# Kernel tuning notes

Measured on AMD Instinct MI355X. Metric: run time of the kernel, lower is better.

## Reference

```python
import jax, jax.numpy as jnp
import numpy as np

TAU = 0.1
HARD_K = 32
MIN_OVERLAP = 4
PAIR_WEIGHTS = [("view", "cart", 0.2), ("cart", "purchase", 1.0), ("view", "purchase", 1.0)]


def setup_inputs() -> dict:
    key = jax.random.key(0)
    ks = jax.random.split(key, 6)
    U, D = 100000, 128
    return {
        "emb_view": jax.random.normal(ks[0], (U, D), dtype=jnp.float32),
        "emb_cart": jax.random.normal(ks[1], (U, D), dtype=jnp.float32),
        "emb_purchase": jax.random.normal(ks[2], (U, D), dtype=jnp.float32),
        "users_view": jax.random.randint(ks[3], (20000,), 0, U, dtype=jnp.int64),
        "users_cart": jax.random.randint(ks[4], (15000,), 0, U, dtype=jnp.int64),
        "users_purchase": jax.random.randint(ks[5], (10000,), 0, U, dtype=jnp.int64),
    }


def _l2norm(x):
    # F.normalize(x, dim=-1): x / max(||x||, eps)
    n = jnp.linalg.norm(x, axis=-1, keepdims=True)
    return x / jnp.maximum(n, 1e-12)


def _directional(z_weak, z_strong, tau, hard_k):
    N = z_strong.shape[0]
    if N < 2:
        return jnp.zeros((), dtype=z_strong.dtype)
    z_w = _l2norm(jax.lax.stop_gradient(z_weak))  # weak side is detached
    z_s = _l2norm(z_strong)
    sim = (z_s @ z_w.T) / tau  # [N, N]
    pos = jnp.diagonal(sim)    # positive logits, labels = arange(N)
    n_hard = min(hard_k, N - 1)
    if 0 < n_hard < N - 1:
        neg_only = jnp.where(jnp.eye(N, dtype=bool), -jnp.inf, sim)
        hard_neg, _ = jax.lax.top_k(neg_only, n_hard)          # [N, n_hard]
        logits = jnp.concatenate([pos[:, None], hard_neg], 1)  # [N, 1+n_hard]
        return jnp.mean(jax.scipy.special.logsumexp(logits, axis=1) - pos)
    # full-softmax CE with label i for row i
    return jnp.mean(jax.scipy.special.logsumexp(sim, axis=1) - pos)


def reference(emb_view, emb_cart, emb_purchase, users_view, users_cart, users_purchase):
    embs = {"view": emb_view, "cart": emb_cart, "purchase": emb_purchase}
    users = {
        "view": np.asarray(users_view),
        "cart": np.asarray(users_cart),
        "purchase": np.asarray(users_purchase),
    }
    loss = jnp.zeros((), dtype=emb_view.dtype)
    for weak, strong, w in PAIR_WEIGHTS:
        u_w, u_s = users[weak], users[strong]
        if u_w.size == 0 or u_s.size == 0:
            continue
        # common_pair = u_w[isin(u_w, u_s)] : keeps u_w order and duplicates
        common = u_w[np.isin(u_w, u_s)]
        if common.size < MIN_OVERLAP:
            continue
        idx = jnp.asarray(common)
        loss = loss + w * _directional(embs[weak][idx], embs[strong][idx], TAU, HARD_K)
    return loss
```

## Files before the change

kernel.cpp:

```cpp
#include <hip/hip_runtime.h>
#include <hip/hip_bf16.h>
#include <math.h>

#define D 128
#define NEG_INF (-3.0e38f)
#define LDA 136
#define MAGIC 0x5CA1AB1Eu

#define C0 3200
#define C1 1792
#define C2 2304
#define T0 25
#define T1 14
#define T2 18
#define NTILES (T0 * T0 + T1 * T1 + T2 * T2)
#define NSEL (C0 / 4 + C1 / 4 + C2 / 4)

typedef __attribute__((ext_vector_type(8))) short bf16x8;
typedef __attribute__((ext_vector_type(8))) unsigned short u16x8;
typedef __attribute__((ext_vector_type(4))) float f32x4;

__device__ __forceinline__ float wredf_add(float v) {
#pragma unroll
  for (int m = 32; m; m >>= 1) v += __shfl_xor(v, m, 64);
  return v;
}
__device__ __forceinline__ float wredf_max(float v) {
#pragma unroll
  for (int m = 32; m; m >>= 1) v = fmaxf(v, __shfl_xor(v, m, 64));
  return v;
}
__device__ __forceinline__ float wredf_min(float v) {
#pragma unroll
  for (int m = 32; m; m >>= 1) v = fminf(v, __shfl_xor(v, m, 64));
  return v;
}
__device__ __forceinline__ int wredi_add(int v) {
#pragma unroll
  for (int m = 32; m; m >>= 1) v += __shfl_xor(v, m, 64);
  return v;
}
__device__ __forceinline__ double wredd_add(double v) {
#pragma unroll
  for (int m = 32; m; m >>= 1) v += __shfl_xor(v, m, 64);
  return v;
}

__global__ void masks_k(const int* __restrict__ uc, int nc,
                        const int* __restrict__ up, int npu,
                        unsigned* __restrict__ mc, unsigned* __restrict__ mp,
                        unsigned long long* __restrict__ header) {
  if (blockIdx.x == 0)
    for (int t = threadIdx.x; t < 1024; t += 256) header[t] = 0ull;
  int t = blockIdx.x * blockDim.x + threadIdx.x;
  if (t < nc) {
    mc[uc[t]] = MAGIC;
  } else {
    int t2 = t - nc;
    if (t2 < npu) mp[up[t2]] = MAGIC;
  }
}

struct FGArgs {
  const int* src[3];
  int n[3];
  const unsigned* mask[3];
  const float* embW[3];
  const float* embS[3];
  short* zw[3];
  short* zs[3];
  int cap[3];
  int seg1, seg2;
  int* counts;
};

__global__ __launch_bounds__(256) void filtgather_k(FGArgs a) {
  int t = blockIdx.x * 256 + threadIdx.x;
  int lane = threadIdx.x & 63;
  int s, base;
  if (t < a.seg1) { s = 0; base = t; }
  else if (t < a.seg2) { s = 1; base = t - a.seg1; }
  else { s = 2; base = t - a.seg2; }
  bool match = false;
  int u = 0;
  if (base < a.n[s]) {
    u = a.src[s][base];
    match = (a.mask[s][u] == MAGIC);
  }
  unsigned long long b = __ballot(match);
  int tot = __popcll(b);
  if (!tot) return;
  int idx0 = 0;
  if (lane == 0) idx0 = atomicAdd(a.counts + s, tot);
  idx0 = __shfl(idx0, 0, 64);
  const float* eW = a.embW[s];
  const float* eS = a.embS[s];
  short* zw = a.zw[s];
  short* zs = a.zs[s];
  int cap = a.cap[s];
  int kmax = tot;
  int rem = cap - idx0;
  if (rem < kmax) kmax = (rem < 0) ? 0 : rem;
  unsigned long long bbL = b;

  auto ldpair = [&](int k, float2& W, float2& S) {
    if (k < kmax) {
      int sl = __builtin_ctzll(bbL);
      bbL &= bbL - 1;
      int uu = __shfl(u, sl, 64);
      W = *(const float2*)(eW + (size_t)uu * D + lane * 2);
      S = *(const float2*)(eS + (size_t)uu * D + lane * 2);
    }
  };
  auto proc = [&](int k, float2 vw, float2 vs) {
    if (k < kmax) {
      int p = idx0 + k;
      float ssw = wredf_add(vw.x * vw.x + vw.y * vw.y);
      float sss = wredf_add(vs.x * vs.x + vs.y * vs.y);
      float iw = 1.0f / fmaxf(sqrtf(ssw), 1e-12f);
      float is = 1.0f / fmaxf(sqrtf(sss), 1e-12f);
      __hip_bfloat16 w0 = __float2bfloat16(vw.x * iw), w1 = __float2bfloat16(vw.y * iw);
      __hip_bfloat16 s0 = __float2bfloat16(vs.x * is), s1 = __float2bfloat16(vs.y * is);
      *(ushort2*)(zw + (size_t)p * D + lane * 2) =
          make_ushort2(*(unsigned short*)&w0, *(unsigned short*)&w1);
      *(ushort2*)(zs + (size_t)p * D + lane * 2) =
          make_ushort2(*(unsigned short*)&s0, *(unsigned short*)&s1);
    }
  };

  float2 Aw0 = {}, Aw1 = {}, Aw2 = {}, Aw3 = {}, Asv0 = {}, Asv1 = {}, Asv2 = {}, Asv3 = {};
  float2 Bw0 = {}, Bw1 = {}, Bw2 = {}, Bw3 = {}, Bsv0 = {}, Bsv1 = {}, Bsv2 = {}, Bsv3 = {};
  int kb = 0;
  ldpair(0, Aw0, Asv0); ldpair(1, Aw1, Asv1); ldpair(2, Aw2, Asv2); ldpair(3, Aw3, Asv3);
  while (kb < kmax) {
    ldpair(kb + 4, Bw0, Bsv0); ldpair(kb + 5, Bw1, Bsv1);
    ldpair(kb + 6, Bw2, Bsv2); ldpair(kb + 7, Bw3, Bsv3);
    proc(kb + 0, Aw0, Asv0); proc(kb + 1, Aw1, Asv1);
    proc(kb + 2, Aw2, Asv2); proc(kb + 3, Aw3, Asv3);
    kb += 4;
    if (kb >= kmax) break;
    ldpair(kb + 4, Aw0, Asv0); ldpair(kb + 5, Aw1, Asv1);
    ldpair(kb + 6, Aw2, Asv2); ldpair(kb + 7, Aw3, Asv3);
    proc(kb + 0, Bw0, Bsv0); proc(kb + 1, Bw1, Bsv1);
    proc(kb + 2, Bw2, Bsv2); proc(kb + 3, Bw3, Bsv3);
    kb += 4;
  }
}

struct GemmArgs {
  const short *zs0, *zw0, *zs1, *zw1, *zs2, *zw2;
  unsigned short *s0, *s1, *s2;
  const int* counts;
};

__device__ __forceinline__ void gemm_tile(const short* __restrict__ A, const short* __restrict__ B,
                                          unsigned short* __restrict__ C, int ldc, int bx, int by,
                                          int N, short* As, short* Bs, int tid) {
  int rb = by * 128, cb = bx * 128;
  if (rb >= N || cb >= N) return;
  int rrow = tid >> 4, rcol = (tid & 15) * 8;
#pragma unroll
  for (int pass = 0; pass < 8; ++pass) {
    int row = pass * 16 + rrow;
    uint4 va = *(const uint4*)(A + (size_t)(rb + row) * D + rcol);
    uint4 vb = *(const uint4*)(B + (size_t)(cb + row) * D + rcol);
    *(uint4*)(&As[row * LDA + rcol]) = va;
    *(uint4*)(&Bs[row * LDA + rcol]) = vb;
  }
  __syncthreads();
  int wave = tid >> 6, lane = tid & 63;
  int wr = (wave >> 1) * 64, wc = (wave & 1) * 64;
  int ln = lane & 15, quad = lane >> 4;
  f32x4 acc[4][4] = {};
#pragma unroll
  for (int ks = 0; ks < 4; ++ks) {
    int ko = ks * 32 + quad * 8;
    bf16x8 af[4], bg[4];
#pragma unroll
    for (int i = 0; i < 4; ++i) af[i] = *(const bf16x8*)(&As[(wr + i * 16 + ln) * LDA + ko]);
#pragma unroll
    for (int j = 0; j < 4; ++j) bg[j] = *(const bf16x8*)(&Bs[(wc + j * 16 + ln) * LDA + ko]);
#pragma unroll
    for (int i = 0; i < 4; ++i)
#pragma unroll
      for (int j = 0; j < 4; ++j)
        acc[i][j] = __builtin_amdgcn_mfma_f32_16x16x32_bf16(af[i], bg[j], acc[i][j], 0, 0, 0);
  }
  __syncthreads();
#pragma unroll
  for (int i = 0; i < 4; ++i)
#pragma unroll
    for (int j = 0; j < 4; ++j) {
      int tcol = wc + j * 16 + ln;
#pragma unroll
      for (int r = 0; r < 4; ++r) {
        int trow = wr + i * 16 + quad * 4 + r;
        __hip_bfloat16 h = __float2bfloat16(acc[i][j][r] * 10.0f);
        As[trow * LDA + tcol] = *(short*)&h;
      }
    }
  __syncthreads();
#pragma unroll
  for (int pass = 0; pass < 8; ++pass) {
    int idx = pass * 256 + tid;
    int row = idx >> 4, c8 = (idx & 15) * 8;
    *(uint4*)(C + (size_t)(rb + row) * ldc + cb + c8) = *(const uint4*)(&As[row * LDA + c8]);
  }
  __syncthreads();
}

__global__ __launch_bounds__(256) void gemm_all_k(GemmArgs g) {
  __shared__ __align__(16) short As[128 * LDA];
  __shared__ __align__(16) short Bs[128 * LDA];
  int tid = threadIdx.x;
  int b = blockIdx.x;
  if (b < T0 * T0) {
    int N = min(g.counts[0], C0);
    gemm_tile(g.zs0, g.zw0, g.s0, C0, b % T0, b / T0, N, As, Bs, tid);
  } else if (b < T0 * T0 + T1 * T1) {
    int t = b - T0 * T0;
    int N = min(g.counts[1], C1);
    gemm_tile(g.zs1, g.zw1, g.s1, C1, t % T1, t / T1, N, As, Bs, tid);
  } else {
    int t = b - T0 * T0 - T1 * T1;
    int N = min(g.counts[2], C2);
    gemm_tile(g.zs2, g.zw2, g.s2, C2, t % T2, t / T2, N, As, Bs, tid);
  }
}

template <int NL>
__device__ __forceinline__ void select_rows(const unsigned short* __restrict__ sim, int ldc, int N,
                                            int i, int lane, double* __restrict__ slot) {
  const unsigned short* row = sim + (size_t)i * ldc;
  float vals[NL * 8];
  float posl = NEG_INF;
#pragma unroll
  for (int L = 0; L < NL; ++L) {
    int base = L * 512 + lane * 8;
    u16x8 raw = *(const u16x8*)(row + base);
#pragma unroll
    for (int c = 0; c < 8; ++c) {
      int j = base + c;
      float v = __uint_as_float((unsigned)raw[c] << 16);
      if (L >= NL - 2 && j >= N) v = NEG_INF;
      if (j == i) { posl = v; v = NEG_INF; }
      vals[L * 8 + c] = v;
    }
  }
  float pos = __shfl(posl, (i >> 3) & 63, 64);
  float m = NEG_INF;
#pragma unroll
  for (int s = 0; s < NL * 8; ++s) m = fmaxf(m, vals[s]);
  m = wredf_max(m);
  int K = min(32, N - 1);
  float lo = -10.2f, hi = m + 1e-3f;
  for (int it = 0; it < 12; ++it) {
    float mid = 0.5f * (lo + hi);
    int c = 0;
#pragma unroll
    for (int s = 0; s < NL * 8; ++s) c += (vals[s] > mid) ? 1 : 0;
    c = wredi_add(c);
    if (c >= K) lo = mid; else hi = mid;
  }
  float M = fmaxf(m, pos);
  float sum = 0.0f, vmin = 3.0e38f;
  int cnt = 0;
#pragma unroll
  for (int s = 0; s < NL * 8; ++s) {
    float v = vals[s];
    if (v > lo) {
      sum += __expf(v - M);
      cnt++;
      vmin = fminf(vmin, v);
    }
  }
  sum = wredf_add(sum);
  cnt = wredi_add(cnt);
  vmin = wredf_min(vmin);
  float corr = (cnt > K) ? (float)(cnt - K) * __expf(vmin - M) : 0.0f;
  float lse = M + __logf(sum - corr + __expf(pos - M));
  if (lane == 0) atomicAdd(slot, (double)(lse - pos));
}

__device__ __forceinline__ void select_body(int b, int wid, int lane,
                                            const unsigned short* __restrict__ sim0,
                                            const unsigned short* __restrict__ sim1,
                                            const unsigned short* __restrict__ sim2,
                                            const int* __restrict__ counts,
                                            double* __restrict__ partials) {
  if (b < C0 / 4) {
    int N = min(counts[0], C0);
    int i = b * 4 + wid;
    if (i < N) {
      double* slot = partials + 0 * 64 + (b & 63);
      if (N <= 3072) select_rows<6>(sim0, C0, N, i, lane, slot);
      else           select_rows<7>(sim0, C0, N, i, lane, slot);
    }
  } else if (b < C0 / 4 + C1 / 4) {
    int bb = b - C0 / 4;
    int N = min(counts[1], C1);
    int i = bb * 4 + wid;
    if (i < N) {
      double* slot = partials + 64 + (bb & 63);
      if (N <= 1536) select_rows<3>(sim1, C1, N, i, lane, slot);
      else           select_rows<4>(sim1, C1, N, i, lane, slot);
    }
  } else {
    int bb = b - C0 / 4 - C1 / 4;
    int N = min(counts[2], C2);
    int i = bb * 4 + wid;
    if (i < N) {
      double* slot = partials + 128 + (bb & 63);
      if (N <= 2048) select_rows<4>(sim2, C2, N, i, lane, slot);
      else           select_rows<5>(sim2, C2, N, i, lane, slot);
    }
  }
}

__global__ __launch_bounds__(256) void select_k(const unsigned short* __restrict__ sim0,
                                                const unsigned short* __restrict__ sim1,
                                                const unsigned short* __restrict__ sim2,
                                                const int* __restrict__ counts,
                                                double* __restrict__ partials,
                                                int* __restrict__ cntC,
                                                float* __restrict__ out) {
  int tid = threadIdx.x, wid = tid >> 6, lane = tid & 63;
  int nb = gridDim.x;
  for (int b = blockIdx.x; b < NSEL; b += nb)
    select_body(b, wid, lane, sim0, sim1, sim2, counts, partials);
  __syncthreads();
  if (tid == 0) {
    __builtin_amdgcn_fence(__ATOMIC_RELEASE, "agent");
    __hip_atomic_fetch_add(&cntC[(blockIdx.x & 63) * 16], 1, __ATOMIC_RELAXED,
                           __HIP_MEMORY_SCOPE_AGENT);
  }
  if (blockIdx.x == 0) {
    if (tid < 64) {
      for (;;) {
        int s = __hip_atomic_load(&cntC[tid * 16], __ATOMIC_RELAXED, __HIP_MEMORY_SCOPE_AGENT);
        s = wredi_add(s);
        if (s >= nb) break;
        __builtin_amdgcn_s_sleep(2);
      }
    }
    __syncthreads();
    if (tid == 0) __builtin_amdgcn_fence(__ATOMIC_ACQUIRE, "agent");
    __syncthreads();
    __shared__ double ps[4];
    double v = (tid < 192)
                   ? __hip_atomic_load(&partials[tid], __ATOMIC_RELAXED, __HIP_MEMORY_SCOPE_AGENT)
                   : 0.0;
    v = wredd_add(v);
    if (lane == 0 && wid < 3) ps[wid] = v;
    __syncthreads();
    if (tid == 0) {
      const float w[3] = {0.2f, 1.0f, 1.0f};
      const int caps[3] = {C0, C1, C2};
      float tot = 0.0f;
      for (int p = 0; p < 3; ++p) {
        int N = min(counts[p], caps[p]);
        if (N >= 4) tot += w[p] * (float)(ps[p] / (double)N);
      }
      out[0] = tot;
    }
  }
}

__global__ void sentinel_k(float* out) {
  if (threadIdx.x == 0 && blockIdx.x == 0) out[0] = -12345.0f;
}

extern "C" void kernel_launch(void* const* d_in, const int* in_sizes, int n_in,
                              void* d_out, int out_size, void* d_ws, size_t ws_size,
                              hipStream_t stream) {
  const float* emb_view = (const float*)d_in[0];
  const float* emb_cart = (const float*)d_in[1];
  const float* emb_pur  = (const float*)d_in[2];
  const int* u_view = (const int*)d_in[3];
  const int* u_cart = (const int*)d_in[4];
  const int* u_pur  = (const int*)d_in[5];
  int nv = in_sizes[3], nc = in_sizes[4], np = in_sizes[5];
  int U = in_sizes[0] / D;

  size_t off = 8192;
  auto alloc = [&](size_t b) {
    size_t o = (off + 255) & ~(size_t)255;
    off = o + b;
    return o;
  };
  size_t mask0_off = alloc((size_t)U * 4);
  size_t mask1_off = alloc((size_t)U * 4);
  size_t zw0_off = alloc((size_t)C0 * D * 2);
  size_t zs0_off = alloc((size_t)C0 * D * 2);
  size_t zw1_off = alloc((size_t)C1 * D * 2);
  size_t zs1_off = alloc((size_t)C1 * D * 2);
  size_t zw2_off = alloc((size_t)C2 * D * 2);
  size_t zs2_off = alloc((size_t)C2 * D * 2);
  size_t sim0_off = alloc((size_t)C0 * C0 * 2);
  size_t sim1_off = alloc((size_t)C1 * C1 * 2);
  size_t sim2_off = alloc((size_t)C2 * C2 * 2);
  (void)alloc(1024);
  int ws_ok = (off <= ws_size) ? 1 : 0;

  char* ws = (char*)d_ws;
  if (!ws_ok) {
    sentinel_k<<<1, 1, 0, stream>>>((float*)d_out);
    return;
  }

  int* counts = (int*)ws;
  int* cntC = (int*)(ws + 1024);
  double* partials = (double*)(ws + 5632);
  unsigned* mask_c = (unsigned*)(ws + mask0_off);
  unsigned* mask_p = (unsigned*)(ws + mask1_off);
  short* zw0 = (short*)(ws + zw0_off);
  short* zs0 = (short*)(ws + zs0_off);
  short* zw1 = (short*)(ws + zw1_off);
  short* zs1 = (short*)(ws + zs1_off);
  short* zw2 = (short*)(ws + zw2_off);
  short* zs2 = (short*)(ws + zs2_off);
  unsigned short* sim0 = (unsigned short*)(ws + sim0_off);
  unsigned short* sim1 = (unsigned short*)(ws + sim1_off);
  unsigned short* sim2 = (unsigned short*)(ws + sim2_off);

  masks_k<<<(nc + np + 255) / 256, 256, 0, stream>>>(u_cart, nc, u_pur, np, mask_c, mask_p,
                                                     (unsigned long long*)ws);

  FGArgs fa;
  fa.src[0] = u_view; fa.n[0] = nv; fa.mask[0] = mask_c;
  fa.embW[0] = emb_view; fa.embS[0] = emb_cart; fa.zw[0] = zw0; fa.zs[0] = zs0; fa.cap[0] = C0;
  fa.src[1] = u_cart; fa.n[1] = nc; fa.mask[1] = mask_p;
  fa.embW[1] = emb_cart; fa.embS[1] = emb_pur; fa.zw[1] = zw1; fa.zs[1] = zs1; fa.cap[1] = C1;
  fa.src[2] = u_view; fa.n[2] = nv; fa.mask[2] = mask_p;
  fa.embW[2] = emb_view; fa.embS[2] = emb_pur; fa.zw[2] = zw2; fa.zs[2] = zs2; fa.cap[2] = C2;
  fa.seg1 = ((nv + 255) / 256) * 256;
  fa.seg2 = fa.seg1 + ((nc + 255) / 256) * 256;
  int t_filt = fa.seg2 + ((nv + 255) / 256) * 256;
  fa.counts = counts;
  filtgather_k<<<t_filt / 256, 256, 0, stream>>>(fa);

  GemmArgs g;
  g.zs0 = zs0; g.zw0 = zw0; g.s0 = sim0;
  g.zs1 = zs1; g.zw1 = zw1; g.s1 = sim1;
  g.zs2 = zs2; g.zw2 = zw2; g.s2 = sim2;
  g.counts = counts;
  gemm_all_k<<<NTILES, 256, 0, stream>>>(g);

  static int s_gC = 0;
  if (s_gC == 0) {
    int nb = 0;
    if (hipOccupancyMaxActiveBlocksPerMultiprocessor(
            &nb, reinterpret_cast<const void*>(select_k), 256, 0) != hipSuccess || nb < 1)
      nb = 1;
    long gsz = (long)nb * 256;
    s_gC = (int)((gsz < NSEL) ? gsz : NSEL);
  }
  select_k<<<s_gC, 256, 0, stream>>>(sim0, sim1, sim2, counts, partials, cntC, (float*)d_out);
}
```

Baseline: 232.9 us.

## Spread gather across block waves, ballot-count bisection, one select block per tile

The filter-gather kernel now gives each block one 64-candidate chunk. The matched rows are split round-robin across the block's 4 waves instead of being processed by a single wave with manual double-buffering, so more waves work on the gather and normalisation. In the top-k threshold bisection, counts now come from wave ballots with popcount instead of per-lane counters followed by a shuffle reduction. The select kernel drops its occupancy-sized persistent grid and launches one block per work item, with the final reducer waiting for all NSEL blocks. This relies on block 0 staying resident while it spins until every other block has finished.

```diff
diff --git a/kernel.cpp b/kernel.cpp
--- a/kernel.cpp
+++ b/kernel.cpp
@@ -75,75 +75,53 @@
 };
 
 __global__ __launch_bounds__(256) void filtgather_k(FGArgs a) {
-  int t = blockIdx.x * 256 + threadIdx.x;
-  int lane = threadIdx.x & 63;
-  int s, base;
-  if (t < a.seg1) { s = 0; base = t; }
-  else if (t < a.seg2) { s = 1; base = t - a.seg1; }
-  else { s = 2; base = t - a.seg2; }
+  int lane = threadIdx.x & 63, w = threadIdx.x >> 6;
+  int cb = blockIdx.x;
+  int s, cand0;
+  if (cb < a.seg1) { s = 0; cand0 = cb * 64; }
+  else if (cb < a.seg2) { s = 1; cand0 = (cb - a.seg1) * 64; }
+  else { s = 2; cand0 = (cb - a.seg2) * 64; }
   bool match = false;
   int u = 0;
-  if (base < a.n[s]) {
-    u = a.src[s][base];
+  int cand = cand0 + lane;
+  if (cand < a.n[s]) {
+    u = a.src[s][cand];
     match = (a.mask[s][u] == MAGIC);
   }
   unsigned long long b = __ballot(match);
   int tot = __popcll(b);
   if (!tot) return;
-  int idx0 = 0;
-  if (lane == 0) idx0 = atomicAdd(a.counts + s, tot);
-  idx0 = __shfl(idx0, 0, 64);
+  __shared__ int sIdx0;
+  if (threadIdx.x == 0) sIdx0 = atomicAdd(a.counts + s, tot);
+  __syncthreads();
+  int idx0 = sIdx0;
+  int cap = a.cap[s];
+  int kmax = tot;
+  int rem = cap - idx0;
+  if (rem < kmax) kmax = (rem < 0) ? 0 : rem;
   const float* eW = a.embW[s];
   const float* eS = a.embS[s];
   short* zw = a.zw[s];
   short* zs = a.zs[s];
-  int cap = a.cap[s];
-  int kmax = tot;
-  int rem = cap - idx0;
-  if (rem < kmax) kmax = (rem < 0) ? 0 : rem;
-  unsigned long long bbL = b;
-
-  auto ldpair = [&](int k, float2& W, float2& S) {
-    if (k < kmax) {
-      int sl = __builtin_ctzll(bbL);
-      bbL &= bbL - 1;
-      int uu = __shfl(u, sl, 64);
-      W = *(const float2*)(eW + (size_t)uu * D + lane * 2);
-      S = *(const float2*)(eS + (size_t)uu * D + lane * 2);
-    }
-  };
-  auto proc = [&](int k, float2 vw, float2 vs) {
-    if (k < kmax) {
-      int p = idx0 + k;
-      float ssw = wredf_add(vw.x * vw.x + vw.y * vw.y);
-      float sss = wredf_add(vs.x * vs.x + vs.y * vs.y);
-      float iw = 1.0f / fmaxf(sqrtf(ssw), 1e-12f);
-      float is = 1.0f / fmaxf(sqrtf(sss), 1e-12f);
-      __hip_bfloat16 w0 = __float2bfloat16(vw.x * iw), w1 = __float2bfloat16(vw.y * iw);
-      __hip_bfloat16 s0 = __float2bfloat16(vs.x * is), s1 = __float2bfloat16(vs.y * is);
-      *(ushort2*)(zw + (size_t)p * D + lane * 2) =
-          make_ushort2(*(unsigned short*)&w0, *(unsigned short*)&w1);
-      *(ushort2*)(zs + (size_t)p * D + lane * 2) =
-          make_ushort2(*(unsigned short*)&s0, *(unsigned short*)&s1);
-    }
-  };
-
-  float2 Aw0 = {}, Aw1 = {}, Aw2 = {}, Aw3 = {}, Asv0 = {}, Asv1 = {}, Asv2 = {}, Asv3 = {};
-  float2 Bw0 = {}, Bw1 = {}, Bw2 = {}, Bw3 = {}, Bsv0 = {}, Bsv1 = {}, Bsv2 = {}, Bsv3 = {};
-  int kb = 0;
-  ldpair(0, Aw0, Asv0); ldpair(1, Aw1, Asv1); ldpair(2, Aw2, Asv2); ldpair(3, Aw3, Asv3);
-  while (kb < kmax) {
-    ldpair(kb + 4, Bw0, Bsv0); ldpair(kb + 5, Bw1, Bsv1);
-    ldpair(kb + 6, Bw2, Bsv2); ldpair(kb + 7, Bw3, Bsv3);
-    proc(kb + 0, Aw0, Asv0); proc(kb + 1, Aw1, Asv1);
-    proc(kb + 2, Aw2, Asv2); proc(kb + 3, Aw3, Asv3);
-    kb += 4;
-    if (kb >= kmax) break;
-    ldpair(kb + 4, Aw0, Asv0); ldpair(kb + 5, Aw1, Asv1);
-    ldpair(kb + 6, Aw2, Asv2); ldpair(kb + 7, Aw3, Asv3);
-    proc(kb + 0, Bw0, Bsv0); proc(kb + 1, Bw1, Bsv1);
-    proc(kb + 2, Bw2, Bsv2); proc(kb + 3, Bw3, Bsv3);
-    kb += 4;
+  unsigned long long bb = b;
+  for (int i = 0; i < w; ++i) bb &= bb - 1;
+  for (int k = w; k < kmax; k += 4) {
+    int sl = __builtin_ctzll(bb);
+    int uu = __shfl(u, sl, 64);
+    int p = idx0 + k;
+    float2 vw = *(const float2*)(eW + (size_t)uu * D + lane * 2);
+    float2 vs = *(const float2*)(eS + (size_t)uu * D + lane * 2);
+    float ssw = wredf_add(vw.x * vw.x + vw.y * vw.y);
+    float sss = wredf_add(vs.x * vs.x + vs.y * vs.y);
+    float iw = 1.0f / fmaxf(sqrtf(ssw), 1e-12f);
+    float is = 1.0f / fmaxf(sqrtf(sss), 1e-12f);
+    __hip_bfloat16 w0 = __float2bfloat16(vw.x * iw), w1 = __float2bfloat16(vw.y * iw);
+    __hip_bfloat16 s0 = __float2bfloat16(vs.x * is), s1 = __float2bfloat16(vs.y * is);
+    *(ushort2*)(zw + (size_t)p * D + lane * 2) =
+        make_ushort2(*(unsigned short*)&w0, *(unsigned short*)&w1);
+    *(ushort2*)(zs + (size_t)p * D + lane * 2) =
+        make_ushort2(*(unsigned short*)&s0, *(unsigned short*)&s1);
+    bb &= bb - 1; bb &= bb - 1; bb &= bb - 1; bb &= bb - 1;
   }
 }
 
@@ -258,8 +236,7 @@
     float mid = 0.5f * (lo + hi);
     int c = 0;
 #pragma unroll
-    for (int s = 0; s < NL * 8; ++s) c += (vals[s] > mid) ? 1 : 0;
-    c = wredi_add(c);
+    for (int s = 0; s < NL * 8; ++s) c += (int)__popcll(__ballot(vals[s] > mid));
     if (c >= K) lo = mid; else hi = mid;
   }
   float M = fmaxf(m, pos);
@@ -268,14 +245,14 @@
 #pragma unroll
   for (int s = 0; s < NL * 8; ++s) {
     float v = vals[s];
-    if (v > lo) {
+    bool sel = (v > lo);
+    cnt += (int)__popcll(__ballot(sel));
+    if (sel) {
       sum += __expf(v - M);
-      cnt++;
       vmin = fminf(vmin, v);
     }
   }
   sum = wredf_add(sum);
-  cnt = wredi_add(cnt);
   vmin = wredf_min(vmin);
   float corr = (cnt > K) ? (float)(cnt - K) * __expf(vmin - M) : 0.0f;
   float lse = M + __logf(sum - corr + __expf(pos - M));
@@ -325,9 +302,7 @@
                                                 int* __restrict__ cntC,
                                                 float* __restrict__ out) {
   int tid = threadIdx.x, wid = tid >> 6, lane = tid & 63;
-  int nb = gridDim.x;
-  for (int b = blockIdx.x; b < NSEL; b += nb)
-    select_body(b, wid, lane, sim0, sim1, sim2, counts, partials);
+  select_body(blockIdx.x, wid, lane, sim0, sim1, sim2, counts, partials);
   __syncthreads();
   if (tid == 0) {
     __builtin_amdgcn_fence(__ATOMIC_RELEASE, "agent");
@@ -339,7 +314,7 @@
       for (;;) {
         int s = __hip_atomic_load(&cntC[tid * 16], __ATOMIC_RELAXED, __HIP_MEMORY_SCOPE_AGENT);
         s = wredi_add(s);
-        if (s >= nb) break;
+        if (s >= NSEL) break;
         __builtin_amdgcn_s_sleep(2);
       }
     }
@@ -433,11 +408,11 @@
   fa.embW[1] = emb_cart; fa.embS[1] = emb_pur; fa.zw[1] = zw1; fa.zs[1] = zs1; fa.cap[1] = C1;
   fa.src[2] = u_view; fa.n[2] = nv; fa.mask[2] = mask_p;
   fa.embW[2] = emb_view; fa.embS[2] = emb_pur; fa.zw[2] = zw2; fa.zs[2] = zs2; fa.cap[2] = C2;
-  fa.seg1 = ((nv + 255) / 256) * 256;
-  fa.seg2 = fa.seg1 + ((nc + 255) / 256) * 256;
-  int t_filt = fa.seg2 + ((nv + 255) / 256) * 256;
+  fa.seg1 = (nv + 63) / 64;
+  fa.seg2 = fa.seg1 + (nc + 63) / 64;
+  int nblk_filt = fa.seg2 + (nv + 63) / 64;
   fa.counts = counts;
-  filtgather_k<<<t_filt / 256, 256, 0, stream>>>(fa);
+  filtgather_k<<<nblk_filt, 256, 0, stream>>>(fa);
 
   GemmArgs g;
   g.zs0 = zs0; g.zw0 = zw0; g.s0 = sim0;
@@ -446,14 +421,5 @@
   g.counts = counts;
   gemm_all_k<<<NTILES, 256, 0, stream>>>(g);
 
-  static int s_gC = 0;
-  if (s_gC == 0) {
-    int nb = 0;
-    if (hipOccupancyMaxActiveBlocksPerMultiprocessor(
-            &nb, reinterpret_cast<const void*>(select_k), 256, 0) != hipSuccess || nb < 1)
-      nb = 1;
-    long gsz = (long)nb * 256;
-    s_gC = (int)((gsz < NSEL) ? gsz : NSEL);
-  }
-  select_k<<<s_gC, 256, 0, stream>>>(sim0, sim1, sim2, counts, partials, cntC, (float*)d_out);
-}
+  select_k<<<NSEL, 256, 0, stream>>>(sim0, sim1, sim2, counts, partials, cntC, (float*)d_out);
+}
```

Result: faster. 210.4 us (-9.7%).
